# Kernel tuning notes

Hardware: AMD Instinct MI355X
Metric: run time of the kernel (lower is better)

## Reference

```python
import jax, jax.numpy as jnp
import numpy as np
import math

E = 512
W = 16


def overlap_and_add(signal, frame_step):
    """signal: [..., frames, frame_length] -> [..., frame_step*(frames-1)+frame_length]."""
    outer = signal.shape[:-2]
    frames, frame_length = signal.shape[-2:]
    subframe_length = math.gcd(frame_length, frame_step)
    subframe_step = frame_step // subframe_length
    subframes_per_frame = frame_length // subframe_length
    output_size = frame_step * (frames - 1) + frame_length
    output_subframes = output_size // subframe_length

    # [B, frames*subframes_per_frame, subframe_length]
    B = int(np.prod(outer)) if outer else 1
    sub = signal.reshape(B, frames * subframes_per_frame, subframe_length)
    # destination subframe index for each source subframe
    idx = (jnp.arange(frames)[:, None] * subframe_step
           + jnp.arange(subframes_per_frame)[None, :]).reshape(-1)
    out = jnp.zeros((B, output_subframes, subframe_length), signal.dtype)
    out = out.at[:, idx, :].add(sub)
    return out.reshape(*outer, output_size)


def setup_inputs() -> dict:
    key = jax.random.key(0)
    k1, k2 = jax.random.split(key)
    mixture_w = jax.random.normal(k1, (8, 2, 16000, E), dtype=jnp.float32)
    # nn.Linear(E, W).weight has shape [W, E]
    basis_weight = jax.random.normal(k2, (W, E), dtype=jnp.float32) * (1.0 / math.sqrt(E))
    return {"mixture_w": mixture_w, "basis_weight": basis_weight}


def reference(mixture_w, basis_weight):
    # est_source: [..., frames, W]
    est_source = jnp.einsum('bckE,wE->bckw', mixture_w, basis_weight)
    return overlap_and_add(est_source, W // 2)
```

## Files before the change

### kernel.cpp

```cpp
#include <hip/hip_runtime.h>


#define FRAMES 16000
#define EDIM 512
#define WDIM 16
#define KC 32
#define NCHUNK (EDIM / KC)
#define ROWS 256
#define LDS_STRIDE (KC + 4)
#define OUT_PER_BC (8 * (FRAMES + 1))

__global__ __launch_bounds__(256, 4)
void decoder_kernel(const float* __restrict__ A,
                    const float* __restrict__ B,
                    float* __restrict__ out)
{
    __shared__ float lds_a[ROWS * LDS_STRIDE];

    const int  t  = threadIdx.x;
    const int  bc = blockIdx.y;
    const long f0 = (long)blockIdx.x * 255 - 1;
    const long f  = f0 + t;
    const bool valid = (f >= 0) && (f < FRAMES);

    const float* Abc = A + (size_t)bc * FRAMES * EDIM;

    const int slot  = t & 7;
    const int rbase = t >> 3;

    size_t rowoff[8];
    #pragma unroll
    for (int i = 0; i < 8; ++i) {
        long fr = f0 + (long)(i * 32 + rbase);
        if (fr < 0) fr = 0;
        if (fr >= FRAMES) fr = FRAMES - 1;
        rowoff[i] = (size_t)fr * EDIM + (size_t)(slot * 4);
    }

    float acc[WDIM];
    #pragma unroll
    for (int w = 0; w < WDIM; ++w) acc[w] = 0.f;

    for (int c = 0; c < NCHUNK; ++c) {
        float4 v[8];
        #pragma unroll
        for (int i = 0; i < 8; ++i)
            v[i] = *(const float4*)(Abc + rowoff[i] + (size_t)(c * KC));
        #pragma unroll
        for (int i = 0; i < 8; ++i) {
            const int r = i * 32 + rbase;
            *(float4*)(&lds_a[r * LDS_STRIDE + slot * 4]) = v[i];
        }
        __syncthreads();

        #pragma unroll
        for (int j = 0; j < 8; ++j) {
            const float4 a = *(const float4*)(&lds_a[t * LDS_STRIDE + j * 4]);
            const float* Bk = B + c * KC + j * 4;
            #pragma unroll
            for (int w = 0; w < WDIM; ++w) {
                float s = acc[w];
                s = fmaf(a.x, Bk[w * EDIM + 0], s);
                s = fmaf(a.y, Bk[w * EDIM + 1], s);
                s = fmaf(a.z, Bk[w * EDIM + 2], s);
                s = fmaf(a.w, Bk[w * EDIM + 3], s);
                acc[w] = s;
            }
        }
        __syncthreads();
    }

    if (!valid) {
        #pragma unroll
        for (int w = 0; w < WDIM; ++w) acc[w] = 0.f;
    }

    #pragma unroll
    for (int i = 0; i < 8; ++i) lds_a[t * 8 + i] = acc[8 + i];
    __syncthreads();

    if (t >= 1 && f >= 0 && f <= FRAMES) {
        float r0[8];
        #pragma unroll
        for (int i = 0; i < 8; ++i) r0[i] = acc[i] + lds_a[(t - 1) * 8 + i];
        float* o = out + (size_t)bc * OUT_PER_BC + (size_t)f * 8;
        *(float4*)(o)     = make_float4(r0[0], r0[1], r0[2], r0[3]);
        *(float4*)(o + 4) = make_float4(r0[4], r0[5], r0[6], r0[7]);
    }
}

extern "C" void kernel_launch(void* const* d_in, const int* in_sizes, int n_in,
                              void* d_out, int out_size, void* d_ws, size_t ws_size,
                              hipStream_t stream) {
    const float* A   = (const float*)d_in[0];
    const float* B   = (const float*)d_in[1];
    float*       out = (float*)d_out;

    dim3 grid(63, 16, 1);
    decoder_kernel<<<grid, dim3(256, 1, 1), 0, stream>>>(A, B, out);
}
```

Measured before the change: 821.6 us.

## Keep basis in registers, split K across lanes with shuffle reduction and ring overlap-add

Restructures the kernel so each wave streams its own range of frames, with lanes splitting the 512-wide dot product and holding their basis slice in registers. Per-frame results are reduced with cross-lane shuffles and overlap-added through a small LDS ring buffer. The goal is to remove the heavy repeated global reads of the basis and the LDS staging of activations. The trade-off is fewer, longer-running waves that rely on software prefetch for latency hiding.

```diff
diff --git a/kernel.cpp b/kernel.cpp
--- a/kernel.cpp
+++ b/kernel.cpp
@@ -2,90 +2,100 @@
 
 
 #define FRAMES 16000
-#define EDIM 512
-#define WDIM 16
-#define KC 32
-#define NCHUNK (EDIM / KC)
-#define ROWS 256
-#define LDS_STRIDE (KC + 4)
-#define OUT_PER_BC (8 * (FRAMES + 1))
+#define EDIM   512
+#define OUTF   16001
+#define OUT_PER_BC 128008
+#define BATCHES 16
+#define OFPW    128
 
-__global__ __launch_bounds__(256, 4)
+__global__ __launch_bounds__(128, 2)
 void decoder_kernel(const float* __restrict__ A,
                     const float* __restrict__ B,
                     float* __restrict__ out)
 {
-    __shared__ float lds_a[ROWS * LDS_STRIDE];
+    const int t   = threadIdx.x;
+    const int wid = t >> 6;
+    const int l   = t & 63;
+    const int wq  = l & 7;
+    const int ksl = l >> 3;
+    const int bc  = blockIdx.y;
+    const int o0  = (blockIdx.x * 2 + wid) * OFPW;
 
-    const int  t  = threadIdx.x;
-    const int  bc = blockIdx.y;
-    const long f0 = (long)blockIdx.x * 255 - 1;
-    const long f  = f0 + t;
-    const bool valid = (f >= 0) && (f < FRAMES);
+    __shared__ float ring[2][16][16];
 
-    const float* Abc = A + (size_t)bc * FRAMES * EDIM;
+    const float4* B4 = (const float4*)B;
+    float4 Bw[2][2][8];
+    #pragma unroll
+    for (int w = 0; w < 2; ++w)
+        #pragma unroll
+        for (int h = 0; h < 2; ++h)
+            #pragma unroll
+            for (int j = 0; j < 8; ++j)
+                Bw[w][h][j] = B4[(2*wq + w) * 128 + ksl*16 + h*8 + j];
 
-    const int slot  = t & 7;
-    const int rbase = t >> 3;
+    const float4* Abc = (const float4*)(A + (size_t)bc * FRAMES * EDIM);
 
-    size_t rowoff[8];
-    #pragma unroll
-    for (int i = 0; i < 8; ++i) {
-        long fr = f0 + (long)(i * 32 + rbase);
-        if (fr < 0) fr = 0;
-        if (fr >= FRAMES) fr = FRAMES - 1;
-        rowoff[i] = (size_t)fr * EDIM + (size_t)(slot * 4);
-    }
+    float4 Abuf[2][8];
 
-    float acc[WDIM];
-    #pragma unroll
-    for (int w = 0; w < WDIM; ++w) acc[w] = 0.f;
+    auto loadHalf = [&](float4* dst, int f, int h) {
+        int fc = f; if (fc < 0) fc = 0; if (fc >= FRAMES) fc = FRAMES - 1;
+        const float4* p = Abc + (size_t)fc * 128 + ksl*16 + h*8;
+        #pragma unroll
+        for (int j = 0; j < 8; ++j) dst[j] = p[j];
+    };
 
-    for (int c = 0; c < NCHUNK; ++c) {
-        float4 v[8];
-        #pragma unroll
-        for (int i = 0; i < 8; ++i)
-            v[i] = *(const float4*)(Abc + rowoff[i] + (size_t)(c * KC));
-        #pragma unroll
-        for (int i = 0; i < 8; ++i) {
-            const int r = i * 32 + rbase;
-            *(float4*)(&lds_a[r * LDS_STRIDE + slot * 4]) = v[i];
-        }
-        __syncthreads();
-
+    auto processFrame = [&](int f) {
+        loadHalf(Abuf[1], f, 1);
+        float acc[2][2] = {{0.f,0.f},{0.f,0.f}};
         #pragma unroll
         for (int j = 0; j < 8; ++j) {
-            const float4 a = *(const float4*)(&lds_a[t * LDS_STRIDE + j * 4]);
-            const float* Bk = B + c * KC + j * 4;
-            #pragma unroll
-            for (int w = 0; w < WDIM; ++w) {
-                float s = acc[w];
-                s = fmaf(a.x, Bk[w * EDIM + 0], s);
-                s = fmaf(a.y, Bk[w * EDIM + 1], s);
-                s = fmaf(a.z, Bk[w * EDIM + 2], s);
-                s = fmaf(a.w, Bk[w * EDIM + 3], s);
-                acc[w] = s;
-            }
+            const float4 a = Abuf[0][j];
+            acc[0][0] = fmaf(a.x, Bw[0][0][j].x, acc[0][0]);
+            acc[0][0] = fmaf(a.y, Bw[0][0][j].y, acc[0][0]);
+            acc[0][0] = fmaf(a.z, Bw[0][0][j].z, acc[0][0]);
+            acc[0][0] = fmaf(a.w, Bw[0][0][j].w, acc[0][0]);
+            acc[1][0] = fmaf(a.x, Bw[1][0][j].x, acc[1][0]);
+            acc[1][0] = fmaf(a.y, Bw[1][0][j].y, acc[1][0]);
+            acc[1][0] = fmaf(a.z, Bw[1][0][j].z, acc[1][0]);
+            acc[1][0] = fmaf(a.w, Bw[1][0][j].w, acc[1][0]);
         }
+        loadHalf(Abuf[0], f + 1, 0);
+        #pragma unroll
+        for (int j = 0; j < 8; ++j) {
+            const float4 a = Abuf[1][j];
+            acc[0][1] = fmaf(a.x, Bw[0][1][j].x, acc[0][1]);
+            acc[0][1] = fmaf(a.y, Bw[0][1][j].y, acc[0][1]);
+            acc[0][1] = fmaf(a.z, Bw[0][1][j].z, acc[0][1]);
+            acc[0][1] = fmaf(a.w, Bw[0][1][j].w, acc[0][1]);
+            acc[1][1] = fmaf(a.x, Bw[1][1][j].x, acc[1][1]);
+            acc[1][1] = fmaf(a.y, Bw[1][1][j].y, acc[1][1]);
+            acc[1][1] = fmaf(a.z, Bw[1][1][j].z, acc[1][1]);
+            acc[1][1] = fmaf(a.w, Bw[1][1][j].w, acc[1][1]);
+        }
+        float r0 = acc[0][0] + acc[0][1];
+        float r1 = acc[1][0] + acc[1][1];
+        r0 += __shfl_xor(r0, 8);   r1 += __shfl_xor(r1, 8);
+        r0 += __shfl_xor(r0, 16);  r1 += __shfl_xor(r1, 16);
+        r0 += __shfl_xor(r0, 32);  r1 += __shfl_xor(r1, 32);
+        if (f < 0 || f >= FRAMES) { r0 = 0.f; r1 = 0.f; }
+        if (ksl == 0) {
+            *(float2*)&ring[wid][f & 15][2*wq] = make_float2(r0, r1);
+        }
+    };
+
+    loadHalf(Abuf[0], o0 - 1, 0);
+    processFrame(o0 - 1);
+
+    for (int b = 0; b < BATCHES; ++b) {
+        const int cf = o0 + b * 8;
+        #pragma unroll
+        for (int r = 0; r < 8; ++r) processFrame(cf + r);
         __syncthreads();
-    }
-
-    if (!valid) {
-        #pragma unroll
-        for (int w = 0; w < WDIM; ++w) acc[w] = 0.f;
-    }
-
-    #pragma unroll
-    for (int i = 0; i < 8; ++i) lds_a[t * 8 + i] = acc[8 + i];
-    __syncthreads();
-
-    if (t >= 1 && f >= 0 && f <= FRAMES) {
-        float r0[8];
-        #pragma unroll
-        for (int i = 0; i < 8; ++i) r0[i] = acc[i] + lds_a[(t - 1) * 8 + i];
-        float* o = out + (size_t)bc * OUT_PER_BC + (size_t)f * 8;
-        *(float4*)(o)     = make_float4(r0[0], r0[1], r0[2], r0[3]);
-        *(float4*)(o + 4) = make_float4(r0[4], r0[5], r0[6], r0[7]);
+        const int fr = cf + (l >> 3);
+        const float v = ring[wid][fr & 15][l & 7]
+                      + ring[wid][(fr - 1) & 15][8 + (l & 7)];
+        if (fr < OUTF)
+            out[(size_t)bc * OUT_PER_BC + (size_t)cf * 8 + l] = v;
     }
 }
 
@@ -97,5 +107,5 @@
     float*       out = (float*)d_out;
 
     dim3 grid(63, 16, 1);
-    decoder_kernel<<<grid, dim3(256, 1, 1), 0, stream>>>(A, B, out);
+    decoder_kernel<<<grid, dim3(128, 1, 1), 0, stream>>>(A, B, out);
 }
```

Measured after the change: 749.1 us. 8.8% less time.
